# Performance work log

Hardware: AMD Instinct MI355X
Metric: run time of the kernel (lower is better)

Reference implementation:

```python
import jax, jax.numpy as jnp
import numpy as np

B, F_IN, NCH, T = 1, 1, 1536, 128
NW = [476, 476, 292]          # wires per plane (face 0)
NC = [10000, 10000, 10000]    # crossings per plane pair (01, 12, 20)
NCROSS = sum(NC)
E = 120000                    # ~4 nearest-neighbor edges per crossing node
N_FEAT_WIRE = 4
OUT_CH = 4
NODE_DIM = 2 * (F_IN + N_FEAT_WIRE) + 3  # = 13, matches GAT input dim


def setup_inputs() -> dict:
    key = jax.random.key(0)
    ks = jax.random.split(key, 18)
    x = jax.random.normal(ks[0], (B, F_IN, NCH, T), jnp.float32)
    chan_p0 = jax.random.randint(ks[1], (NW[0],), 0, NCH, jnp.int32)
    chan_p1 = jax.random.randint(ks[2], (NW[1],), 0, NCH, jnp.int32)
    chan_p2 = jax.random.randint(ks[3], (NW[2],), 0, NCH, jnp.int32)
    gidx_01 = jax.random.randint(ks[4], (NC[0], 2), 0, min(NW[0], NW[1]), jnp.int32)
    gidx_12 = jax.random.randint(ks[5], (NC[1], 2), 0, min(NW[1], NW[2]), jnp.int32)
    gidx_20 = jax.random.randint(ks[6], (NC[2], 2), 0, min(NW[2], NW[0]), jnp.int32)
    ray_01 = jax.random.normal(ks[7], (NC[0], 2), jnp.float32)
    ray_12 = jax.random.normal(ks[8], (NC[1], 2), jnp.float32)
    ray_20 = jax.random.normal(ks[9], (NC[2], 2), jnp.float32)
    edges = jax.random.randint(ks[10], (2, E), 0, NCROSS, jnp.int32)
    W_gat = jax.random.normal(ks[11], (NODE_DIM, OUT_CH), jnp.float32) * 0.1
    a_src = jax.random.normal(ks[12], (OUT_CH,), jnp.float32) * 0.1
    a_dst = jax.random.normal(ks[13], (OUT_CH,), jnp.float32) * 0.1
    b_gat = jnp.zeros((OUT_CH,), jnp.float32)
    W_mlp = jax.random.normal(ks[14], (OUT_CH, 1), jnp.float32) * 0.1
    b_mlp = jnp.zeros((1,), jnp.float32)
    return dict(x=x, chan_p0=chan_p0, chan_p1=chan_p1, chan_p2=chan_p2,
                gidx_01=gidx_01, gidx_12=gidx_12, gidx_20=gidx_20,
                ray_01=ray_01, ray_12=ray_12, ray_20=ray_20, edges=edges,
                W_gat=W_gat, a_src=a_src, a_dst=a_dst, b_gat=b_gat,
                W_mlp=W_mlp, b_mlp=b_mlp)


def _plane_feats(x, chan, plane_id):
    # x: [B,F,C,T] -> per-wire features [B,T,Nw,F+4]:
    # (signal, wire_ident, channel, 0, plane_id) -- mirrors as_wires_f0_pX.
    sig = jnp.transpose(x[:, :, chan, :], (0, 3, 2, 1))  # [B,T,Nw,F]
    nw = chan.shape[0]
    wire_id = jnp.arange(nw, dtype=jnp.float32)
    extra = jnp.stack([wire_id, chan.astype(jnp.float32),
                       jnp.zeros(nw, jnp.float32),
                       jnp.full((nw,), plane_id, jnp.float32)], axis=-1)  # [Nw,4]
    extra = jnp.broadcast_to(extra[None, None], sig.shape[:2] + extra.shape)
    return jnp.concatenate([sig, extra], axis=-1)


def _cross(fA, fB, gidx, rc):
    # crossing node features: wireA feats ++ wireB feats ++ ray xy ++ tick
    n = gidx.shape[0]
    tick = jnp.broadcast_to(jnp.arange(T, dtype=jnp.float32)[None, :, None, None],
                            (B, T, n, 1))
    rcb = jnp.broadcast_to(rc[None, None], (B, T, n, 2))
    return jnp.concatenate([fA[:, :, gidx[:, 0]], fB[:, :, gidx[:, 1]], rcb, tick],
                           axis=-1)  # [B,T,n,13]


def _gat_one(h, a_src, a_dst, src, dst):
    # single-graph, single-head GAT attention + aggregation. h: [N,OUT_CH]
    s = h @ a_src  # [N]
    d = h @ a_dst
    e = jax.nn.leaky_relu(s[src] + d[dst], 0.2)  # [E]
    m = jax.ops.segment_max(e, dst, num_segments=NCROSS)
    m = jnp.where(jnp.isfinite(m), m, 0.0)
    w = jnp.exp(e - m[dst])
    denom = jax.ops.segment_sum(w, dst, num_segments=NCROSS)
    msg = jax.ops.segment_sum(w[:, None] * h[src], dst, num_segments=NCROSS)
    return msg / (denom[:, None] + 1e-9)


def reference(x, chan_p0, chan_p1, chan_p2, gidx_01, gidx_12, gidx_20,
              ray_01, ray_12, ray_20, edges,
              W_gat, a_src, a_dst, b_gat, W_mlp, b_mlp):
    f0 = _plane_feats(x, chan_p0, 0.0)
    f1 = _plane_feats(x, chan_p1, 1.0)
    f2 = _plane_feats(x, chan_p2, 2.0)
    nodes = jnp.concatenate([_cross(f0, f1, gidx_01, ray_01),
                             _cross(f1, f2, gidx_12, ray_12),
                             _cross(f2, f0, gidx_20, ray_20)], axis=2)  # [B,T,N,13]
    h = nodes @ W_gat + b_gat  # [B,T,N,OUT_CH]
    src, dst = edges[0], edges[1]
    gat = jax.vmap(jax.vmap(lambda hh: _gat_one(hh, a_src, a_dst, src, dst)))
    g = gat(h)  # [B,T,N,OUT_CH]
    return jax.nn.sigmoid(g @ W_mlp + b_mlp)  # [B,T,N,1]
```

## Files before the change

kernel.cpp:

```cpp
#include <hip/hip_runtime.h>

#define T_TICKS 128
#define NCH     1536
#define NCPAIR  10000
#define NCROSS  30000
#define E_EDGES 120000
#define TG      4
#define NTG     (T_TICKS / TG)
#define CAP     32
#define BN      256
#define NBLK    ((NCROSS + BN - 1) / BN)
#define NXPOS   (NTG * NCH)
#define PREP_ITEMS (NCROSS + E_EDGES + NXPOS)


__global__ void k_prep(const float* __restrict__ x,
                       const int* __restrict__ c0, const int* __restrict__ c1,
                       const int* __restrict__ c2,
                       const int* __restrict__ g01, const int* __restrict__ g12,
                       const int* __restrict__ g20,
                       const float* __restrict__ r01,
                       const float* __restrict__ r12,
                       const float* __restrict__ r20,
                       const float* __restrict__ Wg,
                       const float* __restrict__ bg,
                       const float* __restrict__ as_,
                       const float* __restrict__ ad_,
                       const float* __restrict__ Wm,
                       const int* __restrict__ e_src,
                       const int* __restrict__ e_dst,
                       int* __restrict__ counts,
                       int* __restrict__ bucket,
                       float4* __restrict__ c4,
                       float* __restrict__ dBv,
                       float4* __restrict__ xT4) {
    const int gid = blockIdx.x * 256 + threadIdx.x;
    if (gid < NCROSS) {
        const int n = gid;
        int iA, iB, m;
        float pA, pB;
        const int* cA;
        const int* cB;
        const float* ray;
        if (n < NCPAIR) {
            m = n; cA = c0; cB = c1; pA = 0.f; pB = 1.f; ray = r01;
            iA = g01[2 * m]; iB = g01[2 * m + 1];
        } else if (n < 2 * NCPAIR) {
            m = n - NCPAIR; cA = c1; cB = c2; pA = 1.f; pB = 2.f; ray = r12;
            iA = g12[2 * m]; iB = g12[2 * m + 1];
        } else {
            m = n - 2 * NCPAIR; cA = c2; cB = c0; pA = 2.f; pB = 0.f; ray = r20;
            iA = g20[2 * m]; iB = g20[2 * m + 1];
        }
        const int chA = cA[iA];
        const int chB = cB[iB];
        const float rx = ray[2 * m];
        const float ry = ray[2 * m + 1];

        float base[4];
#pragma unroll
        for (int c = 0; c < 4; c++) {
            base[c] = bg[c]
                    + (float)iA  * Wg[1 * 4 + c] + (float)chA * Wg[2 * 4 + c]
                    + pA         * Wg[4 * 4 + c]
                    + (float)iB  * Wg[6 * 4 + c] + (float)chB * Wg[7 * 4 + c]
                    + pB         * Wg[9 * 4 + c]
                    + rx         * Wg[10 * 4 + c] + ry * Wg[11 * 4 + c];
        }
        float sB = 0.f, dB = 0.f, pBs = 0.f;
#pragma unroll
        for (int c = 0; c < 4; c++) {
            sB  = fmaf(base[c], as_[c], sB);
            dB  = fmaf(base[c], ad_[c], dB);
            pBs = fmaf(base[c], Wm[c], pBs);
        }
        c4[n]  = make_float4(sB, pBs, __int_as_float(chA), __int_as_float(chB));
        dBv[n] = dB;
    } else if (gid < NCROSS + E_EDGES) {
        const int i = gid - NCROSS;
        const int s = e_src[i];
        const int d = e_dst[i];
        const int slot = atomicAdd(&counts[d], 1);
        if (slot < CAP) bucket[(size_t)d * CAP + slot] = s;
    } else if (gid < PREP_ITEMS) {
        const int i = gid - (NCROSS + E_EDGES);
        const int tg = i / NCH;
        const int c = i - tg * NCH;
        xT4[i] = *(const float4*)(x + c * T_TICKS + tg * TG);
    }
}


__device__ __forceinline__ void upd(float& mx, float& den, float& p,
                                    const float e, const float pj) {
    const float dif = e - mx;
    const float ex = __expf(-fabsf(dif));
    const bool g = dif > 0.f;
    const float scale = g ? ex : 1.f;
    const float w = g ? 1.f : ex;
    mx = g ? e : mx;
    den = fmaf(den, scale, w);
    p = fmaf(p, scale, w * pj);
}

__device__ __forceinline__ void edge_proc(const float4 cs, const float4* xs,
                                          const float sA1, const float sB1,
                                          const float pA1, const float pB1,
                                          const float* ts, const float* tp,
                                          const float* dd,
                                          float* mx, float* den, float* pa) {
    const float4 a4 = xs[__float_as_int(cs.z)];
    const float4 b4 = xs[__float_as_int(cs.w)];
    const float a[4] = {a4.x, a4.y, a4.z, a4.w};
    const float b[4] = {b4.x, b4.y, b4.z, b4.w};
#pragma unroll
    for (int k = 0; k < TG; k++) {
        const float sv = cs.x + a[k] * sA1 + b[k] * sB1 + ts[k];
        const float pv = cs.y + a[k] * pA1 + b[k] * pB1 + tp[k];
        float e = sv + dd[k];
        e = fmaxf(e, 0.2f * e);
        upd(mx[k], den[k], pa[k], e, pv);
    }
}

__global__ __launch_bounds__(BN, 5) void k_gat(
        const float4* __restrict__ xT4,
        const float4* __restrict__ c4,
        const float* __restrict__ dBv,
        const int* __restrict__ counts,
        const int* __restrict__ bucket,
        const float* __restrict__ Wg,
        const float* __restrict__ as_,
        const float* __restrict__ ad_,
        const float* __restrict__ Wm,
        const float* __restrict__ bm,
        float* __restrict__ out) {
    const int lid = blockIdx.x;
    const int xcd = lid & 7;
    const int s   = lid >> 3;
    const int q   = s / NBLK;
    const int nb  = s - q * NBLK;
    const int tg  = xcd + 8 * q;
    const int bbase = nb * BN;
    const int tid = threadIdx.x;
    const int wsz = min(BN, NCROSS - bbase);

    __shared__ float4 xs[NCH];
    __shared__ int perm[BN];
    __shared__ int bins[CAP + 1];
    __shared__ int boff[CAP + 1];
    __shared__ float lres[TG][BN];

    for (int c = tid; c < NCH; c += BN) xs[c] = xT4[tg * NCH + c];

    float sA1 = 0, dA1 = 0, pA1 = 0, sB1 = 0, dB1 = 0, pB1 = 0,
          sT = 0, dT = 0, pT = 0;
#pragma unroll
    for (int c = 0; c < 4; c++) {
        const float va = as_[c], vd = ad_[c], vm = Wm[c];
        const float w0 = Wg[c], w5 = Wg[5 * 4 + c], w12 = Wg[12 * 4 + c];
        sA1 = fmaf(w0, va, sA1);  dA1 = fmaf(w0, vd, dA1);  pA1 = fmaf(w0, vm, pA1);
        sB1 = fmaf(w5, va, sB1);  dB1 = fmaf(w5, vd, dB1);  pB1 = fmaf(w5, vm, pB1);
        sT  = fmaf(w12, va, sT);  dT  = fmaf(w12, vd, dT);  pT  = fmaf(w12, vm, pT);
    }

    int deg0 = 0;
    if (tid < wsz) deg0 = min(counts[bbase + tid], CAP);
    if (tid <= CAP) bins[tid] = 0;
    __syncthreads();
    int lp = 0;
    if (tid < wsz) lp = atomicAdd(&bins[deg0], 1);
    __syncthreads();
    if (tid == 0) {
        int run = 0;
        for (int d = CAP; d >= 0; d--) { boff[d] = run; run += bins[d]; }
    }
    __syncthreads();
    if (tid < wsz) perm[boff[deg0] + lp] = tid | (deg0 << 16);
    __syncthreads();

    if (tid < wsz) {
        const int pk = perm[tid];
        const int nloc = pk & 0xffff;
        const int deg = pk >> 16;
        const int n = bbase + nloc;

        const float4 cc = c4[n];
        const float4 a4 = xs[__float_as_int(cc.z)];
        const float4 b4 = xs[__float_as_int(cc.w)];
        const float dB = dBv[n];
        const float a[4] = {a4.x, a4.y, a4.z, a4.w};
        const float b[4] = {b4.x, b4.y, b4.z, b4.w};

        float dd[TG], ts[TG], tp[TG];
#pragma unroll
        for (int k = 0; k < TG; k++) {
            const float tk = (float)(tg * TG + k);
            dd[k] = dB + a[k] * dA1 + b[k] * dB1 + tk * dT;
            ts[k] = tk * sT;
            tp[k] = tk * pT;
        }
        float mx[TG], den[TG], pa[TG];
#pragma unroll
        for (int k = 0; k < TG; k++) { mx[k] = -INFINITY; den[k] = 0.f; pa[k] = 0.f; }

        const int* bkt = bucket + (size_t)n * CAP;
        for (int j = 0; j < deg; j += 4) {
            const int4 bb = *(const int4*)(bkt + j);
            const int m = deg - j;
            float4 cs0 = c4[bb.x];
            float4 cs1 = make_float4(0.f, 0.f, 0.f, 0.f);
            float4 cs2 = cs1, cs3 = cs1;
            if (m > 1) cs1 = c4[bb.y];
            if (m > 2) cs2 = c4[bb.z];
            if (m > 3) cs3 = c4[bb.w];
            edge_proc(cs0, xs, sA1, sB1, pA1, pB1, ts, tp, dd, mx, den, pa);
            if (m > 1) edge_proc(cs1, xs, sA1, sB1, pA1, pB1, ts, tp, dd, mx, den, pa);
            if (m > 2) edge_proc(cs2, xs, sA1, sB1, pA1, pB1, ts, tp, dd, mx, den, pa);
            if (m > 3) edge_proc(cs3, xs, sA1, sB1, pA1, pB1, ts, tp, dd, mx, den, pa);
        }

        const float bb2 = bm[0];
#pragma unroll
        for (int k = 0; k < TG; k++) {
            const float logit = pa[k] / (den[k] + 1e-9f) + bb2;
            lres[k][nloc] = 1.f / (1.f + __expf(-logit));
        }
    }
    __syncthreads();
    if (tid < wsz) {
#pragma unroll
        for (int k = 0; k < TG; k++) {
            out[(size_t)(tg * TG + k) * NCROSS + bbase + tid] = lres[k][tid];
        }
    }
}


extern "C" void kernel_launch(void* const* d_in, const int* in_sizes, int n_in,
                              void* d_out, int out_size, void* d_ws, size_t ws_size,
                              hipStream_t stream) {
    const float* x   = (const float*)d_in[0];
    const int* c0  = (const int*)d_in[1];
    const int* c1  = (const int*)d_in[2];
    const int* c2  = (const int*)d_in[3];
    const int* g01 = (const int*)d_in[4];
    const int* g12 = (const int*)d_in[5];
    const int* g20 = (const int*)d_in[6];
    const float* r01 = (const float*)d_in[7];
    const float* r12 = (const float*)d_in[8];
    const float* r20 = (const float*)d_in[9];
    const int* edges = (const int*)d_in[10];
    const float* Wg  = (const float*)d_in[11];
    const float* as_ = (const float*)d_in[12];
    const float* ad_ = (const float*)d_in[13];
    const float* bg  = (const float*)d_in[14];
    const float* Wm  = (const float*)d_in[15];
    const float* bm  = (const float*)d_in[16];
    float* out = (float*)d_out;

    const int* e_src = edges;
    const int* e_dst = edges + E_EDGES;

    char* ws = (char*)d_ws;
    size_t off = 0;
    int* counts = (int*)(ws + off); off += NCROSS * sizeof(int);
    off = (off + 255) & ~(size_t)255;
    int* bucket = (int*)(ws + off); off += (size_t)NCROSS * CAP * sizeof(int);
    off = (off + 255) & ~(size_t)255;
    float4* c4 = (float4*)(ws + off); off += (size_t)NCROSS * sizeof(float4);
    off = (off + 255) & ~(size_t)255;
    float* dBv = (float*)(ws + off); off += NCROSS * sizeof(float);
    off = (off + 255) & ~(size_t)255;
    float4* xT4 = (float4*)(ws + off); off += (size_t)NXPOS * sizeof(float4);
    (void)ws_size; (void)n_in; (void)in_sizes; (void)out_size;

    hipMemsetAsync(counts, 0, NCROSS * sizeof(int), stream);

    k_prep<<<(PREP_ITEMS + 255) / 256, 256, 0, stream>>>(
        x, c0, c1, c2, g01, g12, g20, r01, r12, r20, Wg, bg, as_, ad_, Wm,
        e_src, e_dst, counts, bucket, c4, dBv, xT4);

    k_gat<<<NBLK * NTG, BN, 0, stream>>>(xT4, c4, dBv, counts, bucket,
                                         Wg, as_, ad_, Wm, bm, out);
}
```

Baseline: 146.6 us.

## Map four threads per node across tick groups and read x directly from global

The GAT kernel now gives each block 64 nodes and 16 ticks, with four threads per node each owning a group of 4 ticks. The shared-memory staging of a transposed x slice and the xT4 transpose in prep are dropped; x is read with float4 loads straight from global. dB is packed into c4 along with both channel indices, the edge loop is made branch-free by loading all four neighbors unconditionally, and the bin prefix sum is parallelised. This removes the transpose pass and the per-block LDS fill and raises per-thread memory parallelism, at the cost of scattered global/L2 reads of x in place of LDS hits.

```diff
diff --git a/kernel.cpp b/kernel.cpp
--- a/kernel.cpp
+++ b/kernel.cpp
@@ -6,12 +6,12 @@
 #define NCROSS  30000
 #define E_EDGES 120000
 #define TG      4
-#define NTG     (T_TICKS / TG)
+#define TGB     16
+#define NCHUNK  (T_TICKS / TGB)
 #define CAP     32
-#define BN      256
-#define NBLK    ((NCROSS + BN - 1) / BN)
-#define NXPOS   (NTG * NCH)
-#define PREP_ITEMS (NCROSS + E_EDGES + NXPOS)
+#define BNODE   64
+#define NBLKN   ((NCROSS + BNODE - 1) / BNODE)
+#define PREP_ITEMS (NCROSS + E_EDGES)
 
 
 __global__ void k_prep(const float* __restrict__ x,
@@ -31,9 +31,7 @@
                        const int* __restrict__ e_dst,
                        int* __restrict__ counts,
                        int* __restrict__ bucket,
-                       float4* __restrict__ c4,
-                       float* __restrict__ dBv,
-                       float4* __restrict__ xT4) {
+                       float4* __restrict__ c4) {
     const int gid = blockIdx.x * 256 + threadIdx.x;
     if (gid < NCROSS) {
         const int n = gid;
@@ -74,19 +72,13 @@
             dB  = fmaf(base[c], ad_[c], dB);
             pBs = fmaf(base[c], Wm[c], pBs);
         }
-        c4[n]  = make_float4(sB, pBs, __int_as_float(chA), __int_as_float(chB));
-        dBv[n] = dB;
-    } else if (gid < NCROSS + E_EDGES) {
+        c4[n] = make_float4(sB, pBs, dB, __int_as_float(chA | (chB << 16)));
+    } else if (gid < PREP_ITEMS) {
         const int i = gid - NCROSS;
         const int s = e_src[i];
         const int d = e_dst[i];
         const int slot = atomicAdd(&counts[d], 1);
         if (slot < CAP) bucket[(size_t)d * CAP + slot] = s;
-    } else if (gid < PREP_ITEMS) {
-        const int i = gid - (NCROSS + E_EDGES);
-        const int tg = i / NCH;
-        const int c = i - tg * NCH;
-        xT4[i] = *(const float4*)(x + c * T_TICKS + tg * TG);
     }
 }
 
@@ -103,30 +95,26 @@
     p = fmaf(p, scale, w * pj);
 }
 
-__device__ __forceinline__ void edge_proc(const float4 cs, const float4* xs,
+__device__ __forceinline__ void edge_proc(const bool valid, const float4 cs,
+                                          const float4 a4, const float4 b4,
                                           const float sA1, const float sB1,
                                           const float pA1, const float pB1,
-                                          const float* ts, const float* tp,
-                                          const float* dd,
+                                          const float* tp, const float* dm,
                                           float* mx, float* den, float* pa) {
-    const float4 a4 = xs[__float_as_int(cs.z)];
-    const float4 b4 = xs[__float_as_int(cs.w)];
     const float a[4] = {a4.x, a4.y, a4.z, a4.w};
     const float b[4] = {b4.x, b4.y, b4.z, b4.w};
 #pragma unroll
     for (int k = 0; k < TG; k++) {
-        const float sv = cs.x + a[k] * sA1 + b[k] * sB1 + ts[k];
+        float e = cs.x + a[k] * sA1 + b[k] * sB1 + dm[k];
+        e = fmaxf(e, 0.2f * e);
         const float pv = cs.y + a[k] * pA1 + b[k] * pB1 + tp[k];
-        float e = sv + dd[k];
-        e = fmaxf(e, 0.2f * e);
-        upd(mx[k], den[k], pa[k], e, pv);
-    }
-}
-
-__global__ __launch_bounds__(BN, 5) void k_gat(
-        const float4* __restrict__ xT4,
+        if (valid) upd(mx[k], den[k], pa[k], e, pv);
+    }
+}
+
+__global__ __launch_bounds__(256, 4) void k_gat(
+        const float* __restrict__ x,
         const float4* __restrict__ c4,
-        const float* __restrict__ dBv,
         const int* __restrict__ counts,
         const int* __restrict__ bucket,
         const float* __restrict__ Wg,
@@ -136,22 +124,16 @@
         const float* __restrict__ bm,
         float* __restrict__ out) {
     const int lid = blockIdx.x;
-    const int xcd = lid & 7;
-    const int s   = lid >> 3;
-    const int q   = s / NBLK;
-    const int nb  = s - q * NBLK;
-    const int tg  = xcd + 8 * q;
-    const int bbase = nb * BN;
+    const int tgb = lid & 7;
+    const int nb  = lid >> 3;
+    const int bbase = nb * BNODE;
     const int tid = threadIdx.x;
-    const int wsz = min(BN, NCROSS - bbase);
-
-    __shared__ float4 xs[NCH];
-    __shared__ int perm[BN];
+    const int wsz = min(BNODE, NCROSS - bbase);
+
+    __shared__ int perm[BNODE];
     __shared__ int bins[CAP + 1];
     __shared__ int boff[CAP + 1];
-    __shared__ float lres[TG][BN];
-
-    for (int c = tid; c < NCH; c += BN) xs[c] = xT4[tg * NCH + c];
+    __shared__ float lres[TGB][BNODE + 2];
 
     float sA1 = 0, dA1 = 0, pA1 = 0, sB1 = 0, dB1 = 0, pB1 = 0,
           sT = 0, dT = 0, pT = 0;
@@ -171,33 +153,37 @@
     int lp = 0;
     if (tid < wsz) lp = atomicAdd(&bins[deg0], 1);
     __syncthreads();
-    if (tid == 0) {
+    if (tid <= CAP) {
         int run = 0;
-        for (int d = CAP; d >= 0; d--) { boff[d] = run; run += bins[d]; }
+        for (int e = tid + 1; e <= CAP; e++) run += bins[e];
+        boff[tid] = run;
     }
     __syncthreads();
     if (tid < wsz) perm[boff[deg0] + lp] = tid | (deg0 << 16);
     __syncthreads();
 
-    if (tid < wsz) {
-        const int pk = perm[tid];
+    const int nq  = tid >> 2;
+    const int tgl = tid & 3;
+    const int tg  = tgb * 4 + tgl;
+
+    if (nq < wsz) {
+        const int pk = perm[nq];
         const int nloc = pk & 0xffff;
         const int deg = pk >> 16;
         const int n = bbase + nloc;
 
         const float4 cc = c4[n];
-        const float4 a4 = xs[__float_as_int(cc.z)];
-        const float4 b4 = xs[__float_as_int(cc.w)];
-        const float dB = dBv[n];
+        const int cab = __float_as_int(cc.w);
+        const float4 a4 = *(const float4*)(x + (cab & 0xffff) * T_TICKS + tg * TG);
+        const float4 b4 = *(const float4*)(x + (cab >> 16) * T_TICKS + tg * TG);
         const float a[4] = {a4.x, a4.y, a4.z, a4.w};
         const float b[4] = {b4.x, b4.y, b4.z, b4.w};
 
-        float dd[TG], ts[TG], tp[TG];
+        float dm[TG], tp[TG];
 #pragma unroll
         for (int k = 0; k < TG; k++) {
             const float tk = (float)(tg * TG + k);
-            dd[k] = dB + a[k] * dA1 + b[k] * dB1 + tk * dT;
-            ts[k] = tk * sT;
+            dm[k] = cc.z + a[k] * dA1 + b[k] * dB1 + tk * dT + tk * sT;
             tp[k] = tk * pT;
         }
         float mx[TG], den[TG], pa[TG];
@@ -208,30 +194,51 @@
         for (int j = 0; j < deg; j += 4) {
             const int4 bb = *(const int4*)(bkt + j);
             const int m = deg - j;
-            float4 cs0 = c4[bb.x];
-            float4 cs1 = make_float4(0.f, 0.f, 0.f, 0.f);
-            float4 cs2 = cs1, cs3 = cs1;
-            if (m > 1) cs1 = c4[bb.y];
-            if (m > 2) cs2 = c4[bb.z];
-            if (m > 3) cs3 = c4[bb.w];
-            edge_proc(cs0, xs, sA1, sB1, pA1, pB1, ts, tp, dd, mx, den, pa);
-            if (m > 1) edge_proc(cs1, xs, sA1, sB1, pA1, pB1, ts, tp, dd, mx, den, pa);
-            if (m > 2) edge_proc(cs2, xs, sA1, sB1, pA1, pB1, ts, tp, dd, mx, den, pa);
-            if (m > 3) edge_proc(cs3, xs, sA1, sB1, pA1, pB1, ts, tp, dd, mx, den, pa);
+            const int s0 = bb.x;
+            const int s1 = (m > 1) ? bb.y : bb.x;
+            const int s2 = (m > 2) ? bb.z : bb.x;
+            const int s3 = (m > 3) ? bb.w : bb.x;
+            const float4 cs0 = c4[s0];
+            const float4 cs1 = c4[s1];
+            const float4 cs2 = c4[s2];
+            const float4 cs3 = c4[s3];
+            const int i0 = __float_as_int(cs0.w);
+            const int i1 = __float_as_int(cs1.w);
+            const int i2 = __float_as_int(cs2.w);
+            const int i3 = __float_as_int(cs3.w);
+            const float4 xa0 = *(const float4*)(x + (i0 & 0xffff) * T_TICKS + tg * TG);
+            const float4 xb0 = *(const float4*)(x + (i0 >> 16) * T_TICKS + tg * TG);
+            const float4 xa1 = *(const float4*)(x + (i1 & 0xffff) * T_TICKS + tg * TG);
+            const float4 xb1 = *(const float4*)(x + (i1 >> 16) * T_TICKS + tg * TG);
+            const float4 xa2 = *(const float4*)(x + (i2 & 0xffff) * T_TICKS + tg * TG);
+            const float4 xb2 = *(const float4*)(x + (i2 >> 16) * T_TICKS + tg * TG);
+            const float4 xa3 = *(const float4*)(x + (i3 & 0xffff) * T_TICKS + tg * TG);
+            const float4 xb3 = *(const float4*)(x + (i3 >> 16) * T_TICKS + tg * TG);
+            edge_proc(true,  cs0, xa0, xb0, sA1, sB1, pA1, pB1, tp, dm, mx, den, pa);
+            edge_proc(m > 1, cs1, xa1, xb1, sA1, sB1, pA1, pB1, tp, dm, mx, den, pa);
+            edge_proc(m > 2, cs2, xa2, xb2, sA1, sB1, pA1, pB1, tp, dm, mx, den, pa);
+            edge_proc(m > 3, cs3, xa3, xb3, sA1, sB1, pA1, pB1, tp, dm, mx, den, pa);
         }
 
         const float bb2 = bm[0];
 #pragma unroll
         for (int k = 0; k < TG; k++) {
             const float logit = pa[k] / (den[k] + 1e-9f) + bb2;
-            lres[k][nloc] = 1.f / (1.f + __expf(-logit));
-        }
-    }
-    __syncthreads();
-    if (tid < wsz) {
-#pragma unroll
-        for (int k = 0; k < TG; k++) {
-            out[(size_t)(tg * TG + k) * NCROSS + bbase + tid] = lres[k][tid];
+            lres[tgl * 4 + k][nloc] = 1.f / (1.f + __expf(-logit));
+        }
+    }
+    __syncthreads();
+
+    {
+        const int col = tid & 63;
+        const int wv  = tid >> 6;
+        if (col < wsz) {
+#pragma unroll
+            for (int rr = 0; rr < 4; rr++) {
+                const int row = wv * 4 + rr;
+                out[(size_t)(tgb * TGB + row) * NCROSS + bbase + col] =
+                    lres[row][col];
+            }
         }
     }
 }
@@ -269,18 +276,14 @@
     int* bucket = (int*)(ws + off); off += (size_t)NCROSS * CAP * sizeof(int);
     off = (off + 255) & ~(size_t)255;
     float4* c4 = (float4*)(ws + off); off += (size_t)NCROSS * sizeof(float4);
-    off = (off + 255) & ~(size_t)255;
-    float* dBv = (float*)(ws + off); off += NCROSS * sizeof(float);
-    off = (off + 255) & ~(size_t)255;
-    float4* xT4 = (float4*)(ws + off); off += (size_t)NXPOS * sizeof(float4);
     (void)ws_size; (void)n_in; (void)in_sizes; (void)out_size;
 
     hipMemsetAsync(counts, 0, NCROSS * sizeof(int), stream);
 
     k_prep<<<(PREP_ITEMS + 255) / 256, 256, 0, stream>>>(
         x, c0, c1, c2, g01, g12, g20, r01, r12, r20, Wg, bg, as_, ad_, Wm,
-        e_src, e_dst, counts, bucket, c4, dBv, xT4);
-
-    k_gat<<<NBLK * NTG, BN, 0, stream>>>(xT4, c4, dBv, counts, bucket,
-                                         Wg, as_, ad_, Wm, bm, out);
-}
+        e_src, e_dst, counts, bucket, c4);
+
+    k_gat<<<NBLKN * NCHUNK, 256, 0, stream>>>(x, c4, counts, bucket,
+                                              Wg, as_, ad_, Wm, bm, out);
+}
```

Result: faster. 130.4 us (-11.1%).
